# Kernel optimization log

Hardware: AMD Instinct MI355X
Metric: run time of the kernel (lower is better)

Reference implementation:

```python
import jax, jax.numpy as jnp
import numpy as np

NUM_GROUPS = 16
MINIS_PER_GROUP = 16
MINIS_PER_TOK = 4
HIDDEN = 8192
N_TOKENS = 8192


def setup_inputs() -> dict:
    key = jax.random.key(0)
    k1, k2, k3 = jax.random.split(key, 3)
    hidden_states = jax.random.normal(k1, (N_TOKENS, HIDDEN), dtype=jnp.float32)
    # nn.Linear weight: [num_groups, hidden]
    group_gate_w = jax.random.normal(k2, (NUM_GROUPS, HIDDEN), dtype=jnp.float32) * 0.02
    # mini_gates parameter: [num_groups, hidden, minis_per_group]
    mini_gates = jax.random.normal(k3, (NUM_GROUPS, HIDDEN, MINIS_PER_GROUP), dtype=jnp.float32) * 0.02
    return {"hidden_states": hidden_states, "group_gate_w": group_gate_w, "mini_gates": mini_gates}


def reference(hidden_states, group_gate_w, mini_gates):
    # Tier 1: group gate
    group_logits = hidden_states @ group_gate_w.T                      # [N, G]
    group_probs = jax.nn.softmax(group_logits.astype(jnp.float32), axis=-1)
    top_group_probs = jnp.max(group_probs, axis=-1)                    # [N]
    top_group_indices = jnp.argmax(group_probs, axis=-1)               # [N]

    # Tier 2: per-token mini-gate. Instead of gathering a huge [N, H, E]
    # tensor (as the torch code does), compute logits for ALL groups
    # ([N, G, E] is tiny) and select the chosen group's row — same math.
    all_mini_logits = jnp.einsum('nh,ghe->nge', hidden_states, mini_gates)  # [N, G, E]
    mini_logits = jnp.take_along_axis(
        all_mini_logits, top_group_indices[:, None, None], axis=1
    )[:, 0, :]                                                         # [N, E]
    mini_probs = jax.nn.softmax(mini_logits.astype(jnp.float32), axis=-1)

    topk_mini_probs, topk_mini_indices = jax.lax.top_k(mini_probs, MINIS_PER_TOK)
    final_probs = top_group_probs[:, None] * topk_mini_probs
    final_probs = final_probs / jnp.sum(final_probs, axis=-1, keepdims=True)

    global_expert_indices = top_group_indices[:, None] * MINIS_PER_GROUP + topk_mini_indices

    group_aux_loss = jnp.sum(jnp.mean(group_probs, axis=0) ** 2)
    mini_aux_loss = jnp.sum(jnp.mean(mini_probs, axis=0) ** 2)
    total_aux_loss = group_aux_loss + mini_aux_loss

    return (final_probs.astype(hidden_states.dtype), global_expert_indices, total_aux_loss)
```

## Files before the change

kernel.cpp:

```cpp
#include <hip/hip_runtime.h>
#include <math.h>

#define N_TOK 8192
#define HID   8192
#define NG    16
#define NE    16
#define KC    256
#define NCHUNK (HID / KC)
#define TPB   16
#define TPW   2

#define OFF_CNT   0u
#define OFF_GSUM  64u
#define OFF_ESUM  128u
#define OFF_NTIL  192u
#define ZERO_BYTES 256u
#define OFF_BUCK  256u
#define OFF_SCHED (OFF_BUCK + NG*N_TOK*4)
#define OFF_MGT   (OFF_SCHED + 2048*4)

#define RS_ROUND(o, half)                                                 \
  {                                                                       \
    const bool hi_ = (lane & (o)) != 0;                                   \
    _Pragma("unroll")                                                     \
    for (int i_ = 0; i_ < (half); ++i_) {                                 \
      float s_ = hi_ ? acc[i_] : acc[i_ + (half)];                        \
      float r_ = __shfl_xor(s_, (o));                                     \
      acc[i_] = (hi_ ? acc[i_ + (half)] : acc[i_]) + r_;                  \
    }                                                                     \
  }

__global__ __launch_bounds__(512, 4) void k_group(
    const float* __restrict__ hid, const float* __restrict__ gw,
    int* __restrict__ cnt, int* __restrict__ buckets, float* __restrict__ gsum)
{
    const int tid  = threadIdx.x;
    const int lane = tid & 63;
    const int wv   = tid >> 6;
    const int t0   = blockIdx.x * TPB + wv * TPW;
    const float* __restrict__ a0 = hid + (size_t)t0 * HID + 4 * lane;
    const float* __restrict__ w0 = gw + 4 * lane;

    float4 areg[TPW];
    #pragma unroll
    for (int t = 0; t < TPW; ++t)
        areg[t] = *(const float4*)&a0[(size_t)t * HID];

    float acc[32];
    #pragma unroll
    for (int i = 0; i < 32; ++i) acc[i] = 0.f;

    #pragma unroll 1
    for (int c = 0; c < NCHUNK; ++c) {
        const int kb = c * KC;
        float4 aC[TPW];
        #pragma unroll
        for (int t = 0; t < TPW; ++t) aC[t] = areg[t];
        if (c + 1 < NCHUNK) {
            #pragma unroll
            for (int t = 0; t < TPW; ++t)
                areg[t] = *(const float4*)&a0[(size_t)t * HID + kb + KC];
        }
        #pragma unroll
        for (int g = 0; g < NG; ++g) {
            float4 w = *(const float4*)&w0[(size_t)g * HID + kb];
            #pragma unroll
            for (int t = 0; t < TPW; ++t) {
                acc[t*16+g] = fmaf(aC[t].x, w.x, acc[t*16+g]);
                acc[t*16+g] = fmaf(aC[t].y, w.y, acc[t*16+g]);
                acc[t*16+g] = fmaf(aC[t].z, w.z, acc[t*16+g]);
                acc[t*16+g] = fmaf(aC[t].w, w.w, acc[t*16+g]);
            }
        }
        __builtin_amdgcn_s_barrier();
    }

    #pragma unroll
    for (int i = 0; i < 32; ++i) acc[i] += __shfl_xor(acc[i], 32);
    RS_ROUND(16, 16) RS_ROUND(8, 8) RS_ROUND(4, 4) RS_ROUND(2, 2) RS_ROUND(1, 1)
    float v = acc[0];
    float mx = v;
    #pragma unroll
    for (int o = 8; o; o >>= 1) mx = fmaxf(mx, __shfl_xor(mx, o));
    float p = expf(v - mx);
    float s = p;
    #pragma unroll
    for (int o = 8; o; o >>= 1) s += __shfl_xor(s, o);
    p /= s;
    float x = p;
    x += __shfl_xor(x, 16);
    if (lane < 16) unsafeAtomicAdd(&gsum[lane], x);
    int gi = lane & 15; float bv = v;
    #pragma unroll
    for (int o = 8; o; o >>= 1) {
        float ov = __shfl_xor(bv, o);
        int   og = __shfl_xor(gi, o);
        if (ov > bv || (ov == bv && og < gi)) { bv = ov; gi = og; }
    }
    if (lane < 32 && (lane & 15) == 0) {
        int t = t0 + (lane >> 4);
        int pos = atomicAdd(&cnt[gi], 1);
        buckets[gi * N_TOK + pos] = t;
    }
}

__global__ __launch_bounds__(256) void k_tr(
    const float* __restrict__ mg, float* __restrict__ mgT)
{
    const int g  = blockIdx.x >> 7;
    const int kb = (blockIdx.x & 127) * 64;
    const int e  = threadIdx.x & 15;
    const int kq = threadIdx.x >> 4;
    const int k0 = kb + 4 * kq;
    const float* src = mg + (size_t)g * HID * NE;
    float4 v;
    v.x = src[(size_t)(k0 + 0) * NE + e];
    v.y = src[(size_t)(k0 + 1) * NE + e];
    v.z = src[(size_t)(k0 + 2) * NE + e];
    v.w = src[(size_t)(k0 + 3) * NE + e];
    *(float4*)&mgT[(size_t)(g * NE + e) * HID + k0] = v;
}

__global__ void k_sched(const int* __restrict__ cnt, int* __restrict__ sched,
                        int* __restrict__ ntile)
{
    __shared__ int pref[NG + 1];
    if (threadIdx.x == 0) {
        int s = 0;
        for (int g = 0; g < NG; ++g) { pref[g] = s; s += (cnt[g] + TPB - 1) / TPB; }
        pref[NG] = s; *ntile = s;
    }
    __syncthreads();
    int total = pref[NG];
    for (int i = threadIdx.x; i < total; i += blockDim.x) {
        int g = 0;
        while (g < NG - 1 && i >= pref[g + 1]) ++g;
        sched[i] = (g << 16) | (i - pref[g]);
    }
}

__global__ __launch_bounds__(512, 4) void k_mini(
    const float* __restrict__ hid, const float* __restrict__ mgT,
    const int* __restrict__ cnt, const int* __restrict__ buckets,
    const int* __restrict__ sched, const int* __restrict__ ntile,
    float* __restrict__ out, float* __restrict__ esum)
{
    if ((int)blockIdx.x >= *ntile) return;
    const int enc  = sched[blockIdx.x];
    const int g    = enc >> 16;
    const int tile = enc & 0xffff;
    const int n    = cnt[g] - tile * TPB;

    __shared__ int   rows[TPB];
    __shared__ float sm[256];
    const int tid  = threadIdx.x;
    const int lane = tid & 63;
    const int wv   = tid >> 6;
    const float* __restrict__ w0 = mgT + (size_t)g * NE * HID + 4 * lane;

    if (tid < TPB)
        rows[tid] = buckets[g * N_TOK + tile * TPB + min(tid, n - 1)];
    __syncthreads();
    const float* at[TPW];
    #pragma unroll
    for (int t = 0; t < TPW; ++t)
        at[t] = hid + (size_t)rows[wv * TPW + t] * HID + 4 * lane;

    float4 areg[TPW];
    #pragma unroll
    for (int t = 0; t < TPW; ++t)
        areg[t] = *(const float4*)&at[t][0];

    float acc[32];
    #pragma unroll
    for (int i = 0; i < 32; ++i) acc[i] = 0.f;

    #pragma unroll 1
    for (int c = 0; c < NCHUNK; ++c) {
        const int kb = c * KC;
        float4 aC[TPW];
        #pragma unroll
        for (int t = 0; t < TPW; ++t) aC[t] = areg[t];
        if (c + 1 < NCHUNK) {
            #pragma unroll
            for (int t = 0; t < TPW; ++t)
                areg[t] = *(const float4*)&at[t][kb + KC];
        }
        #pragma unroll
        for (int e = 0; e < NE; ++e) {
            float4 w = *(const float4*)&w0[(size_t)e * HID + kb];
            #pragma unroll
            for (int t = 0; t < TPW; ++t) {
                acc[t*16+e] = fmaf(aC[t].x, w.x, acc[t*16+e]);
                acc[t*16+e] = fmaf(aC[t].y, w.y, acc[t*16+e]);
                acc[t*16+e] = fmaf(aC[t].z, w.z, acc[t*16+e]);
                acc[t*16+e] = fmaf(aC[t].w, w.w, acc[t*16+e]);
            }
        }
        __builtin_amdgcn_s_barrier();
    }

    #pragma unroll
    for (int i = 0; i < 32; ++i) acc[i] += __shfl_xor(acc[i], 32);
    RS_ROUND(16, 16) RS_ROUND(8, 8) RS_ROUND(4, 4) RS_ROUND(2, 2) RS_ROUND(1, 1)
    const int tl = wv * TPW + ((lane >> 4) & 1);
    float v = acc[0];
    float mx = v;
    #pragma unroll
    for (int o = 8; o; o >>= 1) mx = fmaxf(mx, __shfl_xor(mx, o));
    float p = expf(v - mx);
    float s = p;
    #pragma unroll
    for (int o = 8; o; o >>= 1) s += __shfl_xor(s, o);
    p /= s;
    float x = (tl < n) ? p : 0.f;
    x += __shfl_xor(x, 16);
    if (lane < 16) unsafeAtomicAdd(&esum[lane], x);

    if (lane < 32) sm[tl * 16 + (lane & 15)] = p;
    __syncthreads();
    if (tid < 256 && (tid & 15) == 0) {
        int tt = tid >> 4;
        if (tt < n) {
            float pe[NE];
            #pragma unroll
            for (int e = 0; e < NE; ++e) pe[e] = sm[tt * 16 + e];
            unsigned used = 0;
            float tv[4]; int ti[4];
            #pragma unroll
            for (int j = 0; j < 4; ++j) {
                float best = -1.f; int bi = 0;
                #pragma unroll
                for (int e = 0; e < NE; ++e)
                    if (!((used >> e) & 1u) && pe[e] > best) { best = pe[e]; bi = e; }
                used |= 1u << bi; tv[j] = best; ti[j] = bi;
            }
            float inv4 = 1.f / (tv[0] + tv[1] + tv[2] + tv[3]);
            int t = rows[tt];
            #pragma unroll
            for (int j = 0; j < 4; ++j) {
                out[t * 4 + j]             = tv[j] * inv4;
                out[N_TOK * 4 + t * 4 + j] = (float)(g * NE + ti[j]);
            }
        }
    }
}

__global__ void k_aux(const float* __restrict__ gsum, const float* __restrict__ esum,
                      float* __restrict__ out)
{
    if (threadIdx.x == 0) {
        float a = 0.f;
        for (int g = 0; g < NG; ++g) { float m = gsum[g] * (1.f / N_TOK); a += m * m; }
        for (int e = 0; e < NE; ++e) { float m = esum[e] * (1.f / N_TOK); a += m * m; }
        out[N_TOK * 8] = a;
    }
}

extern "C" void kernel_launch(void* const* d_in, const int* in_sizes, int n_in,
                              void* d_out, int out_size, void* d_ws, size_t ws_size,
                              hipStream_t stream) {
    const float* hid = (const float*)d_in[0];
    const float* gw  = (const float*)d_in[1];
    const float* mg  = (const float*)d_in[2];
    float* out = (float*)d_out;
    char*  ws  = (char*)d_ws;
    int*    cnt     = (int*)   (ws + OFF_CNT);
    float*  gsum    = (float*) (ws + OFF_GSUM);
    float*  esum    = (float*) (ws + OFF_ESUM);
    int*    ntile   = (int*)   (ws + OFF_NTIL);
    int*    buckets = (int*)   (ws + OFF_BUCK);
    int*    sched   = (int*)   (ws + OFF_SCHED);
    float*  mgT     = (float*) (ws + OFF_MGT);

    hipMemsetAsync(d_ws, 0, ZERO_BYTES, stream);

    k_tr<<<2048, 256, 0, stream>>>(mg, mgT);
    k_group<<<N_TOK / TPB, 512, 0, stream>>>(hid, gw, cnt, buckets, gsum);
    k_sched<<<1, 256, 0, stream>>>(cnt, sched, ntile);
    k_mini<<<N_TOK / TPB + NG, 512, 0, stream>>>(hid, mgT, cnt, buckets, sched, ntile, out, esum);
    k_aux<<<1, 64, 0, stream>>>(gsum, esum, out);
}
```

Before: 589.1 us.

## Stage gate weights in LDS via async loads and raise tokens per wave

Both the group and mini gate GEMV kernels now stream each 256-wide weight chunk into double-buffered shared memory with global_load_lds, and all waves read it from LDS instead of each wave fetching the weights from global memory. Each wave now handles four tokens instead of two, using 256-thread blocks and 64 accumulators, so each weight read is reused across more tokens. Activation loads are double-buffered in registers across the unrolled chunk pair, with explicit waitcnt and barriers. This costs more registers and fewer waves in flight, and relies on the hand-written vmcnt count being right.

New measurement: 678.5 us. 1.15x slower.

```diff
diff --git a/kernel.cpp b/kernel.cpp
--- a/kernel.cpp
+++ b/kernel.cpp
@@ -8,7 +8,7 @@
 #define KC    256
 #define NCHUNK (HID / KC)
 #define TPB   16
-#define TPW   2
+#define TPW   4
 
 #define OFF_CNT   0u
 #define OFF_GSUM  64u
@@ -18,6 +18,12 @@
 #define OFF_BUCK  256u
 #define OFF_SCHED (OFF_BUCK + NG*N_TOK*4)
 #define OFF_MGT   (OFF_SCHED + 2048*4)
+
+__device__ __forceinline__ void glds16(const float* gp, float* lp) {
+    __builtin_amdgcn_global_load_lds(
+        (const __attribute__((address_space(1))) void*)gp,
+        (__attribute__((address_space(3))) void*)lp, 16, 0, 0);
+}
 
 #define RS_ROUND(o, half)                                                 \
   {                                                                       \
@@ -30,54 +36,71 @@
     }                                                                     \
   }
 
-__global__ __launch_bounds__(512, 4) void k_group(
+#define GBODY(c, ACOMP, ALOAD, WB)                                        \
+  {                                                                       \
+    asm volatile("s_waitcnt vmcnt(4)" ::: "memory");                      \
+    __builtin_amdgcn_s_barrier();                                         \
+    __builtin_amdgcn_sched_barrier(0);                                    \
+    if ((c) + 1 < NCHUNK) {                                               \
+      const int kn_ = ((c) + 1) * KC;                                     \
+      _Pragma("unroll")                                                   \
+      for (int j_ = 0; j_ < 4; ++j_)                                      \
+        glds16(WB + (size_t)(wv * 4 + j_) * HID + kn_ + 4 * lane,         \
+               &Wl[((c) + 1) & 1][(wv * 4 + j_) * KC]);                   \
+      __builtin_amdgcn_sched_barrier(0);                                  \
+      _Pragma("unroll")                                                   \
+      for (int t_ = 0; t_ < TPW; ++t_)                                    \
+        ALOAD[t_] = *(const float4*)&at[t_][kn_];                         \
+    }                                                                     \
+    const float* Wc_ = &Wl[(c) & 1][0];                                   \
+    _Pragma("unroll")                                                     \
+    for (int g_ = 0; g_ < NG; ++g_) {                                     \
+      float4 w_ = *(const float4*)&Wc_[g_ * KC + 4 * lane];               \
+      _Pragma("unroll")                                                   \
+      for (int t_ = 0; t_ < TPW; ++t_) {                                  \
+        acc[t_*16+g_] = fmaf(ACOMP[t_].x, w_.x, acc[t_*16+g_]);           \
+        acc[t_*16+g_] = fmaf(ACOMP[t_].y, w_.y, acc[t_*16+g_]);           \
+        acc[t_*16+g_] = fmaf(ACOMP[t_].z, w_.z, acc[t_*16+g_]);           \
+        acc[t_*16+g_] = fmaf(ACOMP[t_].w, w_.w, acc[t_*16+g_]);           \
+      }                                                                   \
+    }                                                                     \
+  }
+
+__global__ __launch_bounds__(256, 3) void k_group(
     const float* __restrict__ hid, const float* __restrict__ gw,
     int* __restrict__ cnt, int* __restrict__ buckets, float* __restrict__ gsum)
 {
+    __shared__ float Wl[2][NG * KC];
     const int tid  = threadIdx.x;
     const int lane = tid & 63;
     const int wv   = tid >> 6;
     const int t0   = blockIdx.x * TPB + wv * TPW;
-    const float* __restrict__ a0 = hid + (size_t)t0 * HID + 4 * lane;
-    const float* __restrict__ w0 = gw + 4 * lane;
-
-    float4 areg[TPW];
-    #pragma unroll
-    for (int t = 0; t < TPW; ++t)
-        areg[t] = *(const float4*)&a0[(size_t)t * HID];
-
-    float acc[32];
-    #pragma unroll
-    for (int i = 0; i < 32; ++i) acc[i] = 0.f;
+
+    #pragma unroll
+    for (int j = 0; j < 4; ++j)
+        glds16(gw + (size_t)(wv * 4 + j) * HID + 4 * lane, &Wl[0][(wv * 4 + j) * KC]);
+    __builtin_amdgcn_sched_barrier(0);
+
+    const float* at[TPW];
+    #pragma unroll
+    for (int t = 0; t < TPW; ++t) at[t] = hid + (size_t)(t0 + t) * HID + 4 * lane;
+
+    float4 aregA[TPW], aregB[TPW];
+    #pragma unroll
+    for (int t = 0; t < TPW; ++t) aregA[t] = *(const float4*)&at[t][0];
+
+    float acc[64];
+    #pragma unroll
+    for (int i = 0; i < 64; ++i) acc[i] = 0.f;
 
     #pragma unroll 1
-    for (int c = 0; c < NCHUNK; ++c) {
-        const int kb = c * KC;
-        float4 aC[TPW];
-        #pragma unroll
-        for (int t = 0; t < TPW; ++t) aC[t] = areg[t];
-        if (c + 1 < NCHUNK) {
-            #pragma unroll
-            for (int t = 0; t < TPW; ++t)
-                areg[t] = *(const float4*)&a0[(size_t)t * HID + kb + KC];
-        }
-        #pragma unroll
-        for (int g = 0; g < NG; ++g) {
-            float4 w = *(const float4*)&w0[(size_t)g * HID + kb];
-            #pragma unroll
-            for (int t = 0; t < TPW; ++t) {
-                acc[t*16+g] = fmaf(aC[t].x, w.x, acc[t*16+g]);
-                acc[t*16+g] = fmaf(aC[t].y, w.y, acc[t*16+g]);
-                acc[t*16+g] = fmaf(aC[t].z, w.z, acc[t*16+g]);
-                acc[t*16+g] = fmaf(aC[t].w, w.w, acc[t*16+g]);
-            }
-        }
-        __builtin_amdgcn_s_barrier();
-    }
-
-    #pragma unroll
-    for (int i = 0; i < 32; ++i) acc[i] += __shfl_xor(acc[i], 32);
-    RS_ROUND(16, 16) RS_ROUND(8, 8) RS_ROUND(4, 4) RS_ROUND(2, 2) RS_ROUND(1, 1)
+    for (int c = 0; c < NCHUNK; c += 2) {
+        GBODY(c,     aregA, aregB, gw)
+        GBODY(c + 1, aregB, aregA, gw)
+    }
+
+    RS_ROUND(32, 32) RS_ROUND(16, 16) RS_ROUND(8, 8)
+    RS_ROUND(4, 4)   RS_ROUND(2, 2)   RS_ROUND(1, 1)
     float v = acc[0];
     float mx = v;
     #pragma unroll
@@ -89,6 +112,7 @@
     p /= s;
     float x = p;
     x += __shfl_xor(x, 16);
+    x += __shfl_xor(x, 32);
     if (lane < 16) unsafeAtomicAdd(&gsum[lane], x);
     int gi = lane & 15; float bv = v;
     #pragma unroll
@@ -97,7 +121,7 @@
         int   og = __shfl_xor(gi, o);
         if (ov > bv || (ov == bv && og < gi)) { bv = ov; gi = og; }
     }
-    if (lane < 32 && (lane & 15) == 0) {
+    if ((lane & 15) == 0) {
         int t = t0 + (lane >> 4);
         int pos = atomicAdd(&cnt[gi], 1);
         buckets[gi * N_TOK + pos] = t;
@@ -139,7 +163,7 @@
     }
 }
 
-__global__ __launch_bounds__(512, 4) void k_mini(
+__global__ __launch_bounds__(256, 3) void k_mini(
     const float* __restrict__ hid, const float* __restrict__ mgT,
     const int* __restrict__ cnt, const int* __restrict__ buckets,
     const int* __restrict__ sched, const int* __restrict__ ntile,
@@ -151,59 +175,43 @@
     const int tile = enc & 0xffff;
     const int n    = cnt[g] - tile * TPB;
 
+    __shared__ float Wl[2][NE * KC];
     __shared__ int   rows[TPB];
     __shared__ float sm[256];
     const int tid  = threadIdx.x;
     const int lane = tid & 63;
     const int wv   = tid >> 6;
-    const float* __restrict__ w0 = mgT + (size_t)g * NE * HID + 4 * lane;
-
+    const float* __restrict__ wg = mgT + (size_t)g * NE * HID;
+
+    #pragma unroll
+    for (int j = 0; j < 4; ++j)
+        glds16(wg + (size_t)(wv * 4 + j) * HID + 4 * lane, &Wl[0][(wv * 4 + j) * KC]);
     if (tid < TPB)
         rows[tid] = buckets[g * N_TOK + tile * TPB + min(tid, n - 1)];
     __syncthreads();
+
     const float* at[TPW];
     #pragma unroll
     for (int t = 0; t < TPW; ++t)
         at[t] = hid + (size_t)rows[wv * TPW + t] * HID + 4 * lane;
 
-    float4 areg[TPW];
-    #pragma unroll
-    for (int t = 0; t < TPW; ++t)
-        areg[t] = *(const float4*)&at[t][0];
-
-    float acc[32];
-    #pragma unroll
-    for (int i = 0; i < 32; ++i) acc[i] = 0.f;
+    float4 aregA[TPW], aregB[TPW];
+    #pragma unroll
+    for (int t = 0; t < TPW; ++t) aregA[t] = *(const float4*)&at[t][0];
+
+    float acc[64];
+    #pragma unroll
+    for (int i = 0; i < 64; ++i) acc[i] = 0.f;
 
     #pragma unroll 1
-    for (int c = 0; c < NCHUNK; ++c) {
-        const int kb = c * KC;
-        float4 aC[TPW];
-        #pragma unroll
-        for (int t = 0; t < TPW; ++t) aC[t] = areg[t];
-        if (c + 1 < NCHUNK) {
-            #pragma unroll
-            for (int t = 0; t < TPW; ++t)
-                areg[t] = *(const float4*)&at[t][kb + KC];
-        }
-        #pragma unroll
-        for (int e = 0; e < NE; ++e) {
-            float4 w = *(const float4*)&w0[(size_t)e * HID + kb];
-            #pragma unroll
-            for (int t = 0; t < TPW; ++t) {
-                acc[t*16+e] = fmaf(aC[t].x, w.x, acc[t*16+e]);
-                acc[t*16+e] = fmaf(aC[t].y, w.y, acc[t*16+e]);
-                acc[t*16+e] = fmaf(aC[t].z, w.z, acc[t*16+e]);
-                acc[t*16+e] = fmaf(aC[t].w, w.w, acc[t*16+e]);
-            }
-        }
-        __builtin_amdgcn_s_barrier();
-    }
-
-    #pragma unroll
-    for (int i = 0; i < 32; ++i) acc[i] += __shfl_xor(acc[i], 32);
-    RS_ROUND(16, 16) RS_ROUND(8, 8) RS_ROUND(4, 4) RS_ROUND(2, 2) RS_ROUND(1, 1)
-    const int tl = wv * TPW + ((lane >> 4) & 1);
+    for (int c = 0; c < NCHUNK; c += 2) {
+        GBODY(c,     aregA, aregB, wg)
+        GBODY(c + 1, aregB, aregA, wg)
+    }
+
+    RS_ROUND(32, 32) RS_ROUND(16, 16) RS_ROUND(8, 8)
+    RS_ROUND(4, 4)   RS_ROUND(2, 2)   RS_ROUND(1, 1)
+    const int tl = wv * TPW + (lane >> 4);
     float v = acc[0];
     float mx = v;
     #pragma unroll
@@ -215,11 +223,12 @@
     p /= s;
     float x = (tl < n) ? p : 0.f;
     x += __shfl_xor(x, 16);
+    x += __shfl_xor(x, 32);
     if (lane < 16) unsafeAtomicAdd(&esum[lane], x);
 
-    if (lane < 32) sm[tl * 16 + (lane & 15)] = p;
+    sm[tid] = p;
     __syncthreads();
-    if (tid < 256 && (tid & 15) == 0) {
+    if ((tid & 15) == 0) {
         int tt = tid >> 4;
         if (tt < n) {
             float pe[NE];
@@ -276,8 +285,8 @@
     hipMemsetAsync(d_ws, 0, ZERO_BYTES, stream);
 
     k_tr<<<2048, 256, 0, stream>>>(mg, mgT);
-    k_group<<<N_TOK / TPB, 512, 0, stream>>>(hid, gw, cnt, buckets, gsum);
+    k_group<<<N_TOK / TPB, 256, 0, stream>>>(hid, gw, cnt, buckets, gsum);
     k_sched<<<1, 256, 0, stream>>>(cnt, sched, ntile);
-    k_mini<<<N_TOK / TPB + NG, 512, 0, stream>>>(hid, mgT, cnt, buckets, sched, ntile, out, esum);
+    k_mini<<<N_TOK / TPB + NG, 256, 0, stream>>>(hid, mgT, cnt, buckets, sched, ntile, out, esum);
     k_aux<<<1, 64, 0, stream>>>(gsum, esum, out);
 }
```
